# Kernel tuning notes

Measured on AMD Instinct MI355X. Metric: run time of the kernel, lower is better.

Reference implementation:

```python
import jax, jax.numpy as jnp
import numpy as np

TREND_SCALING = 0.6
DETAIL_PRESERVATION = 0.85
SPIKE_THRESHOLD = 3.5
SPIKE_DAMPING = 0.35
ITERATIONS = 2
BASE_WINDOW = 5
STRIDE = max(1, BASE_WINDOW // 2)  # 2
R = BASE_WINDOW                    # 5
EPS = 1e-6


def setup_inputs() -> dict:
    key = jax.random.key(0)
    B, C, L = 4, 4, 1048576
    x = jax.random.normal(key, (B, C, L), dtype=jnp.float32)
    # registered buffers: normalized box kernels (1/window)
    detail_kernel = jnp.ones((1, 1, BASE_WINDOW), jnp.float32) / float(BASE_WINDOW)
    trend_kernel = jnp.ones((1, 1, BASE_WINDOW * 2 + 1), jnp.float32) / float(BASE_WINDOW * 2 + 1)
    return {"x": x, "detail_kernel": detail_kernel, "trend_kernel": trend_kernel}


def _smooth(x, kernel):
    # depthwise (grouped) conv1d with reflect padding, same length out
    pad = kernel.shape[-1] // 2
    xp = jnp.pad(x, ((0, 0), (0, 0), (pad, pad)), mode="reflect")
    C = x.shape[1]
    w = jnp.broadcast_to(kernel, (C, 1, kernel.shape[-1]))
    return jax.lax.conv_general_dilated(
        xp, w, window_strides=(1,), padding="VALID",
        dimension_numbers=("NCH", "OIH", "NCH"), feature_group_count=C)


def _denoise_pass(x, detail_kernel, trend_kernel):
    B, C, L = x.shape
    trend = _smooth(x, trend_kernel)
    local = _smooth(x, detail_kernel)
    residual = x - local
    # torch .std() is unbiased (ddof=1)
    scale = jnp.maximum(jnp.std(residual, axis=-1, keepdims=True, ddof=1), EPS)
    threshold = scale * SPIKE_THRESHOLD
    residual = jnp.where(jnp.abs(residual) > threshold, residual * SPIKE_DAMPING, residual)
    residual = residual * DETAIL_PRESERVATION
    blended = (1.0 - TREND_SCALING) * local + TREND_SCALING * trend
    xp = blended + residual

    remainder = (L - R) % STRIDE
    pad_right = 0 if remainder == 0 else STRIDE - remainder
    if pad_right > 0:
        xp = jnp.pad(xp, ((0, 0), (0, 0), (0, pad_right)), mode="reflect")
    L_pad = xp.shape[-1]

    # overlap-add scatter-mean (faithful to torch unfold + scatter_add_ + count)
    n_ranges = (L_pad - R) // STRIDE + 1
    starts = jnp.arange(n_ranges) * STRIDE                      # [N]
    idx = (starts[:, None] + jnp.arange(R)[None, :]).reshape(-1)  # [N*R]
    xf = xp.reshape(B * C, L_pad)
    segments = xf[:, idx]                                       # [BC, N*R] unfold windows
    out = jnp.zeros((B * C, L_pad), xf.dtype).at[:, idx].add(segments)
    count = jnp.zeros((L_pad,), xf.dtype).at[idx].add(1.0)
    out = out / jnp.maximum(count, 1.0)[None, :]
    return out.reshape(B, C, L_pad)[:, :, :L]


def reference(x, detail_kernel, trend_kernel):
    cur = x.astype(jnp.float32)
    for _ in range(ITERATIONS):
        cur = _denoise_pass(cur, detail_kernel, trend_kernel)
    return cur.astype(x.dtype)
```

## Files before the change

### kernel.cpp

```cpp
#include <hip/hip_runtime.h>

#define NTHREADS 256
#define EPT      8
#define CHUNK    (NTHREADS*EPT)
#define ROWS     16
#define BPRB     64
#define NBLOCKS  (ROWS*BPRB)

#define C_TREND   0.6f
#define C_DETAIL  0.85f
#define C_SPIKE_T 3.5f
#define C_SPIKE_D 0.35f
#define C_EPS     1e-6f

typedef float vfloat4 __attribute__((ext_vector_type(4)));

__device__ __forceinline__ float reflect_load(const float* __restrict__ rp, int g, int L) {
    if (g < 0) g = -g;
    else if (g >= L) g = 2 * L - 2 - g;
    return rp[g];
}

__device__ __forceinline__ void blk_reduce2(double& s, double& s2) {
    #pragma unroll
    for (int off = 32; off > 0; off >>= 1) {
        s  += __shfl_xor(s, off);
        s2 += __shfl_xor(s2, off);
    }
    __shared__ double lds[8];
    int wid = threadIdx.x >> 6, lane = threadIdx.x & 63;
    if (lane == 0) { lds[2*wid] = s; lds[2*wid+1] = s2; }
    __syncthreads();
    s  = lds[0] + lds[2] + lds[4] + lds[6];
    s2 = lds[1] + lds[3] + lds[5] + lds[7];
}

__device__ __forceinline__ float compute_thr(const double2* __restrict__ prow, int L) {
    __shared__ float thr_s;
    if (threadIdx.x < 64) {
        double2 v = prow[threadIdx.x];
        double s = v.x, s2 = v.y;
        #pragma unroll
        for (int off = 32; off > 0; off >>= 1) {
            s  += __shfl_xor(s, off);
            s2 += __shfl_xor(s2, off);
        }
        if (threadIdx.x == 0) {
            double n = (double)L;
            double var = (s2 - s * s / n) / (n - 1.0);
            float stdv = (float)sqrt(fmax(var, 0.0));
            thr_s = fmaxf(stdv, C_EPS) * C_SPIKE_T;
        }
    }
    __syncthreads();
    return thr_s;
}

__device__ float xp1_scalar(const float* __restrict__ rp, int L, int p, float thr) {
    if (p < 0) p = -p;
    else if (p >= L) p = 2 * L - 2 - p;
    float s5 = 0.f, s11 = 0.f;
    #pragma unroll
    for (int k = -5; k <= 5; ++k) {
        float v = reflect_load(rp, p + k, L);
        s11 += v;
        if (k >= -2 && k <= 2) s5 += v;
    }
    float local = s5 * 0.2f;
    float trend = s11 * (1.0f / 11.0f);
    float r = rp[p] - local;
    r = (fabsf(r) > thr) ? r * C_SPIKE_D : r;
    return (1.0f - C_TREND) * local + C_TREND * trend + C_DETAIL * r;
}

__global__ __launch_bounds__(NTHREADS) void k1_reduce(
    const float* __restrict__ x, double2* __restrict__ partials1, int L, int cpb) {
    int row = blockIdx.x / BPRB, cgid = blockIdx.x % BPRB;
    const float* rp = x + (size_t)row * L;
    int base = cgid * cpb;

    double s = 0.0, s2 = 0.0;
    for (int i = 0; i < cpb; ++i) {
        int o = (base + i) * CHUNK + threadIdx.x * EPT;
        float w[16];
        if (o >= 4 && o + 12 <= L) {
            const float4* p = reinterpret_cast<const float4*>(rp + o - 4);
            #pragma unroll
            for (int j = 0; j < 4; ++j) {
                float4 v = p[j];
                w[4*j+0] = v.x; w[4*j+1] = v.y; w[4*j+2] = v.z; w[4*j+3] = v.w;
            }
        } else {
            #pragma unroll
            for (int j = 0; j < 16; ++j) w[j] = reflect_load(rp, o - 4 + j, L);
        }
        float s5 = w[2] + w[3] + w[4] + w[5] + w[6];
        #pragma unroll
        for (int k = 0; k < EPT; ++k) {
            float r = w[4 + k] - s5 * 0.2f;
            s += (double)r;
            s2 = fma((double)r, (double)r, s2);
            if (k < EPT - 1) s5 += w[7 + k] - w[2 + k];
        }
    }
    blk_reduce2(s, s2);
    if (threadIdx.x == 0) partials1[blockIdx.x] = make_double2(s, s2);
}

__global__ __launch_bounds__(NTHREADS) void k2_reduce(
    const float* __restrict__ x, const double2* __restrict__ partials1,
    double2* __restrict__ partials2, int L, int cpb) {
    int row = blockIdx.x / BPRB, cgid = blockIdx.x % BPRB;
    const float* rp = x + (size_t)row * L;
    float t1 = compute_thr(partials1 + row * BPRB, L);
    int base = cgid * cpb;

    double s = 0.0, s2 = 0.0;
    for (int i = 0; i < cpb; ++i) {
        int o = (base + i) * CHUNK + threadIdx.x * EPT;
        float xv[12];
        if (o >= 8 && o + 16 <= L) {
            float w[24];
            const float4* p = reinterpret_cast<const float4*>(rp + o - 8);
            #pragma unroll
            for (int j = 0; j < 6; ++j) {
                float4 v = p[j];
                w[4*j+0] = v.x; w[4*j+1] = v.y; w[4*j+2] = v.z; w[4*j+3] = v.w;
            }
            float s5  = w[4] + w[5] + w[6] + w[7] + w[8];
            float s11 = w[1] + w[2] + w[3] + w[4] + w[5] + w[6]
                      + w[7] + w[8] + w[9] + w[10] + w[11];
            #pragma unroll
            for (int j = 0; j < 12; ++j) {
                float local = s5 * 0.2f;
                float trend = s11 * (1.0f / 11.0f);
                float r = w[6 + j] - local;
                r = (fabsf(r) > t1) ? r * C_SPIKE_D : r;
                xv[j] = (1.0f - C_TREND) * local + C_TREND * trend + C_DETAIL * r;
                if (j < 11) { s5 += w[9 + j] - w[4 + j]; s11 += w[12 + j] - w[1 + j]; }
            }
        } else {
            #pragma unroll
            for (int j = 0; j < 12; ++j) xv[j] = xp1_scalar(rp, L, o - 2 + j, t1);
        }
        float t5 = xv[0] + xv[1] + xv[2] + xv[3] + xv[4];
        #pragma unroll
        for (int k = 0; k < EPT; ++k) {
            float r2 = xv[2 + k] - t5 * 0.2f;
            s += (double)r2;
            s2 = fma((double)r2, (double)r2, s2);
            if (k < EPT - 1) t5 += xv[5 + k] - xv[k];
        }
    }
    blk_reduce2(s, s2);
    if (threadIdx.x == 0) partials2[blockIdx.x] = make_double2(s, s2);
}

__global__ __launch_bounds__(NTHREADS) void k3_apply(
    const float* __restrict__ x, const double2* __restrict__ partials1,
    const double2* __restrict__ partials2, float* __restrict__ out, int L, int cpb) {
    int row = blockIdx.x / BPRB, cgid = blockIdx.x % BPRB;
    const float* rp = x + (size_t)row * L;
    float* orow = out + (size_t)row * L;
    float t1 = compute_thr(partials1 + row * BPRB, L);
    float t2 = compute_thr(partials2 + row * BPRB, L);
    int base = cgid * cpb;

    for (int i = 0; i < cpb; ++i) {
        int o = (base + i) * CHUNK + threadIdx.x * EPT;
        float xv[18];
        if (o >= 12 && o + 20 <= L) {
            float w[32];
            const float4* p = reinterpret_cast<const float4*>(rp + o - 12);
            #pragma unroll
            for (int j = 0; j < 8; ++j) {
                float4 v = p[j];
                w[4*j+0] = v.x; w[4*j+1] = v.y; w[4*j+2] = v.z; w[4*j+3] = v.w;
            }
            float s5  = w[5] + w[6] + w[7] + w[8] + w[9];
            float s11 = w[2] + w[3] + w[4] + w[5] + w[6] + w[7]
                      + w[8] + w[9] + w[10] + w[11] + w[12];
            #pragma unroll
            for (int j = 0; j < 18; ++j) {
                float local = s5 * 0.2f;
                float trend = s11 * (1.0f / 11.0f);
                float r = w[7 + j] - local;
                r = (fabsf(r) > t1) ? r * C_SPIKE_D : r;
                xv[j] = (1.0f - C_TREND) * local + C_TREND * trend + C_DETAIL * r;
                if (j < 17) { s5 += w[10 + j] - w[5 + j]; s11 += w[13 + j] - w[2 + j]; }
            }
        } else {
            #pragma unroll
            for (int j = 0; j < 18; ++j) xv[j] = xp1_scalar(rp, L, o - 5 + j, t1);
        }

        float s5  = xv[3] + xv[4] + xv[5] + xv[6] + xv[7];
        float s11 = xv[0] + xv[1] + xv[2] + xv[3] + xv[4] + xv[5]
                  + xv[6] + xv[7] + xv[8] + xv[9] + xv[10];
        float res[EPT];
        #pragma unroll
        for (int k = 0; k < EPT; ++k) {
            float local = s5 * 0.2f;
            float trend = s11 * (1.0f / 11.0f);
            float r = xv[5 + k] - local;
            r = (fabsf(r) > t2) ? r * C_SPIKE_D : r;
            res[k] = (1.0f - C_TREND) * local + C_TREND * trend + C_DETAIL * r;
            if (k < EPT - 1) { s5 += xv[8 + k] - xv[3 + k]; s11 += xv[11 + k] - xv[k]; }
        }
        vfloat4 r0 = { res[0], res[1], res[2], res[3] };
        vfloat4 r1 = { res[4], res[5], res[6], res[7] };
        __builtin_nontemporal_store(r0, reinterpret_cast<vfloat4*>(orow + o));
        __builtin_nontemporal_store(r1, reinterpret_cast<vfloat4*>(orow + o) + 1);
    }
}

extern "C" void kernel_launch(void* const* d_in, const int* in_sizes, int n_in,
                              void* d_out, int out_size, void* d_ws, size_t ws_size,
                              hipStream_t stream) {
    const float* x = (const float*)d_in[0];
    float* outp = (float*)d_out;

    int total = in_sizes[0];
    int L = total / ROWS;
    int bpr = L / CHUNK;
    int cpb = bpr / BPRB;

    double2* partials1 = (double2*)d_ws;
    double2* partials2 = partials1 + NBLOCKS;

    k1_reduce<<<NBLOCKS, NTHREADS, 0, stream>>>(x, partials1, L, cpb);
    k2_reduce<<<NBLOCKS, NTHREADS, 0, stream>>>(x, partials1, partials2, L, cpb);
    k3_apply <<<NBLOCKS, NTHREADS, 0, stream>>>(x, partials1, partials2, outp, L, cpb);
}
```

Measured before the change: 70.82 us.

## Fuse three passes into one cooperative kernel with grid-wide syncs

Replaces the three separate launches (two statistics reductions and the apply pass) with a single cooperative kernel of 512 blocks that uses grid.sync between phases, with the three-kernel path kept as a fallback. Partials are exchanged through relaxed agent-scope atomic loads and stores. The aim is to remove launch gaps and inter-kernel drain/fill costs. In exchange it runs half as many blocks, each with more chunks, and pays for grid barriers and an occupancy query on every launch.

```diff
diff --git a/kernel.cpp b/kernel.cpp
--- a/kernel.cpp
+++ b/kernel.cpp
@@ -1,11 +1,16 @@
 #include <hip/hip_runtime.h>
+#include <hip/hip_cooperative_groups.h>
+
+namespace cg = cooperative_groups;
 
 #define NTHREADS 256
 #define EPT      8
 #define CHUNK    (NTHREADS*EPT)
 #define ROWS     16
-#define BPRB     64
-#define NBLOCKS  (ROWS*BPRB)
+#define NBLOCKS_C 512
+#define BPRB_C   (NBLOCKS_C/ROWS)
+#define NBLOCKS_F 1024
+#define BPRB_F   (NBLOCKS_F/ROWS)
 
 #define C_TREND   0.6f
 #define C_DETAIL  0.85f
@@ -29,19 +34,28 @@
     }
     __shared__ double lds[8];
     int wid = threadIdx.x >> 6, lane = threadIdx.x & 63;
+    __syncthreads();
     if (lane == 0) { lds[2*wid] = s; lds[2*wid+1] = s2; }
     __syncthreads();
     s  = lds[0] + lds[2] + lds[4] + lds[6];
     s2 = lds[1] + lds[3] + lds[5] + lds[7];
 }
 
-__device__ __forceinline__ float compute_thr(const double2* __restrict__ prow, int L) {
+template<int NPART, bool ATOMIC>
+__device__ __forceinline__ float compute_thr(const double* __restrict__ prow, int L) {
     __shared__ float thr_s;
-    if (threadIdx.x < 64) {
-        double2 v = prow[threadIdx.x];
-        double s = v.x, s2 = v.y;
-        #pragma unroll
-        for (int off = 32; off > 0; off >>= 1) {
+    __syncthreads();
+    if (threadIdx.x < NPART) {
+        double s, s2;
+        if (ATOMIC) {
+            s  = __hip_atomic_load(prow + 2*threadIdx.x + 0, __ATOMIC_RELAXED, __HIP_MEMORY_SCOPE_AGENT);
+            s2 = __hip_atomic_load(prow + 2*threadIdx.x + 1, __ATOMIC_RELAXED, __HIP_MEMORY_SCOPE_AGENT);
+        } else {
+            s  = prow[2*threadIdx.x + 0];
+            s2 = prow[2*threadIdx.x + 1];
+        }
+        #pragma unroll
+        for (int off = NPART/2; off > 0; off >>= 1) {
             s  += __shfl_xor(s, off);
             s2 += __shfl_xor(s2, off);
         }
@@ -73,145 +87,194 @@
     return (1.0f - C_TREND) * local + C_TREND * trend + C_DETAIL * r;
 }
 
+
+__device__ __forceinline__ void chunkA(const float* __restrict__ rp, int o, int L,
+                                       double& s, double& s2) {
+    float w[16];
+    if (o >= 4 && o + 12 <= L) {
+        const float4* p = reinterpret_cast<const float4*>(rp + o - 4);
+        #pragma unroll
+        for (int j = 0; j < 4; ++j) {
+            float4 v = p[j];
+            w[4*j+0] = v.x; w[4*j+1] = v.y; w[4*j+2] = v.z; w[4*j+3] = v.w;
+        }
+    } else {
+        #pragma unroll
+        for (int j = 0; j < 16; ++j) w[j] = reflect_load(rp, o - 4 + j, L);
+    }
+    float s5 = w[2] + w[3] + w[4] + w[5] + w[6];
+    #pragma unroll
+    for (int k = 0; k < EPT; ++k) {
+        float r = w[4 + k] - s5 * 0.2f;
+        s += (double)r;
+        s2 = fma((double)r, (double)r, s2);
+        if (k < EPT - 1) s5 += w[7 + k] - w[2 + k];
+    }
+}
+
+__device__ __forceinline__ void chunkB(const float* __restrict__ rp, int o, int L,
+                                       float t1, double& s, double& s2) {
+    float xv[12];
+    if (o >= 8 && o + 16 <= L) {
+        float w[24];
+        const float4* p = reinterpret_cast<const float4*>(rp + o - 8);
+        #pragma unroll
+        for (int j = 0; j < 6; ++j) {
+            float4 v = p[j];
+            w[4*j+0] = v.x; w[4*j+1] = v.y; w[4*j+2] = v.z; w[4*j+3] = v.w;
+        }
+        float s5  = w[4] + w[5] + w[6] + w[7] + w[8];
+        float s11 = w[1] + w[2] + w[3] + w[4] + w[5] + w[6]
+                  + w[7] + w[8] + w[9] + w[10] + w[11];
+        #pragma unroll
+        for (int j = 0; j < 12; ++j) {
+            float local = s5 * 0.2f;
+            float trend = s11 * (1.0f / 11.0f);
+            float r = w[6 + j] - local;
+            r = (fabsf(r) > t1) ? r * C_SPIKE_D : r;
+            xv[j] = (1.0f - C_TREND) * local + C_TREND * trend + C_DETAIL * r;
+            if (j < 11) { s5 += w[9 + j] - w[4 + j]; s11 += w[12 + j] - w[1 + j]; }
+        }
+    } else {
+        #pragma unroll
+        for (int j = 0; j < 12; ++j) xv[j] = xp1_scalar(rp, L, o - 2 + j, t1);
+    }
+    float t5 = xv[0] + xv[1] + xv[2] + xv[3] + xv[4];
+    #pragma unroll
+    for (int k = 0; k < EPT; ++k) {
+        float r2 = xv[2 + k] - t5 * 0.2f;
+        s += (double)r2;
+        s2 = fma((double)r2, (double)r2, s2);
+        if (k < EPT - 1) t5 += xv[5 + k] - xv[k];
+    }
+}
+
+__device__ __forceinline__ void chunkC(const float* __restrict__ rp, float* __restrict__ orow,
+                                       int o, int L, float t1, float t2) {
+    float xv[18];
+    if (o >= 12 && o + 20 <= L) {
+        float w[32];
+        const float4* p = reinterpret_cast<const float4*>(rp + o - 12);
+        #pragma unroll
+        for (int j = 0; j < 8; ++j) {
+            float4 v = p[j];
+            w[4*j+0] = v.x; w[4*j+1] = v.y; w[4*j+2] = v.z; w[4*j+3] = v.w;
+        }
+        float s5  = w[5] + w[6] + w[7] + w[8] + w[9];
+        float s11 = w[2] + w[3] + w[4] + w[5] + w[6] + w[7]
+                  + w[8] + w[9] + w[10] + w[11] + w[12];
+        #pragma unroll
+        for (int j = 0; j < 18; ++j) {
+            float local = s5 * 0.2f;
+            float trend = s11 * (1.0f / 11.0f);
+            float r = w[7 + j] - local;
+            r = (fabsf(r) > t1) ? r * C_SPIKE_D : r;
+            xv[j] = (1.0f - C_TREND) * local + C_TREND * trend + C_DETAIL * r;
+            if (j < 17) { s5 += w[10 + j] - w[5 + j]; s11 += w[13 + j] - w[2 + j]; }
+        }
+    } else {
+        #pragma unroll
+        for (int j = 0; j < 18; ++j) xv[j] = xp1_scalar(rp, L, o - 5 + j, t1);
+    }
+    float s5  = xv[3] + xv[4] + xv[5] + xv[6] + xv[7];
+    float s11 = xv[0] + xv[1] + xv[2] + xv[3] + xv[4] + xv[5]
+              + xv[6] + xv[7] + xv[8] + xv[9] + xv[10];
+    float res[EPT];
+    #pragma unroll
+    for (int k = 0; k < EPT; ++k) {
+        float local = s5 * 0.2f;
+        float trend = s11 * (1.0f / 11.0f);
+        float r = xv[5 + k] - local;
+        r = (fabsf(r) > t2) ? r * C_SPIKE_D : r;
+        res[k] = (1.0f - C_TREND) * local + C_TREND * trend + C_DETAIL * r;
+        if (k < EPT - 1) { s5 += xv[8 + k] - xv[3 + k]; s11 += xv[11 + k] - xv[k]; }
+    }
+    vfloat4 r0 = { res[0], res[1], res[2], res[3] };
+    vfloat4 r1 = { res[4], res[5], res[6], res[7] };
+    __builtin_nontemporal_store(r0, reinterpret_cast<vfloat4*>(orow + o));
+    __builtin_nontemporal_store(r1, reinterpret_cast<vfloat4*>(orow + o) + 1);
+}
+
+__global__ __launch_bounds__(NTHREADS) void fractal_coop(
+    const float* __restrict__ x, float* __restrict__ out,
+    double* __restrict__ p1, double* __restrict__ p2, int L) {
+    cg::grid_group grid = cg::this_grid();
+    int row  = blockIdx.x / BPRB_C;
+    int cgid = blockIdx.x % BPRB_C;
+    int cpb  = (L / CHUNK) / BPRB_C;
+    const float* rp = x + (size_t)row * L;
+    float* orow = out + (size_t)row * L;
+    int base = cgid * cpb;
+
+    {
+        double s = 0.0, s2 = 0.0;
+        for (int i = 0; i < cpb; ++i)
+            chunkA(rp, (base + i) * CHUNK + threadIdx.x * EPT, L, s, s2);
+        blk_reduce2(s, s2);
+        if (threadIdx.x == 0) {
+            __hip_atomic_store(p1 + 2*blockIdx.x + 0, s,  __ATOMIC_RELAXED, __HIP_MEMORY_SCOPE_AGENT);
+            __hip_atomic_store(p1 + 2*blockIdx.x + 1, s2, __ATOMIC_RELAXED, __HIP_MEMORY_SCOPE_AGENT);
+        }
+    }
+    grid.sync();
+
+    float t1 = compute_thr<BPRB_C, true>(p1 + row * 2 * BPRB_C, L);
+
+    {
+        double s = 0.0, s2 = 0.0;
+        for (int i = 0; i < cpb; ++i)
+            chunkB(rp, (base + i) * CHUNK + threadIdx.x * EPT, L, t1, s, s2);
+        blk_reduce2(s, s2);
+        if (threadIdx.x == 0) {
+            __hip_atomic_store(p2 + 2*blockIdx.x + 0, s,  __ATOMIC_RELAXED, __HIP_MEMORY_SCOPE_AGENT);
+            __hip_atomic_store(p2 + 2*blockIdx.x + 1, s2, __ATOMIC_RELAXED, __HIP_MEMORY_SCOPE_AGENT);
+        }
+    }
+    grid.sync();
+
+    float t2 = compute_thr<BPRB_C, true>(p2 + row * 2 * BPRB_C, L);
+
+    for (int i = 0; i < cpb; ++i)
+        chunkC(rp, orow, (base + i) * CHUNK + threadIdx.x * EPT, L, t1, t2);
+}
+
 __global__ __launch_bounds__(NTHREADS) void k1_reduce(
-    const float* __restrict__ x, double2* __restrict__ partials1, int L, int cpb) {
-    int row = blockIdx.x / BPRB, cgid = blockIdx.x % BPRB;
+    const float* __restrict__ x, double* __restrict__ partials1, int L, int cpb) {
+    int row = blockIdx.x / BPRB_F, cgid = blockIdx.x % BPRB_F;
     const float* rp = x + (size_t)row * L;
     int base = cgid * cpb;
-
     double s = 0.0, s2 = 0.0;
-    for (int i = 0; i < cpb; ++i) {
-        int o = (base + i) * CHUNK + threadIdx.x * EPT;
-        float w[16];
-        if (o >= 4 && o + 12 <= L) {
-            const float4* p = reinterpret_cast<const float4*>(rp + o - 4);
-            #pragma unroll
-            for (int j = 0; j < 4; ++j) {
-                float4 v = p[j];
-                w[4*j+0] = v.x; w[4*j+1] = v.y; w[4*j+2] = v.z; w[4*j+3] = v.w;
-            }
-        } else {
-            #pragma unroll
-            for (int j = 0; j < 16; ++j) w[j] = reflect_load(rp, o - 4 + j, L);
-        }
-        float s5 = w[2] + w[3] + w[4] + w[5] + w[6];
-        #pragma unroll
-        for (int k = 0; k < EPT; ++k) {
-            float r = w[4 + k] - s5 * 0.2f;
-            s += (double)r;
-            s2 = fma((double)r, (double)r, s2);
-            if (k < EPT - 1) s5 += w[7 + k] - w[2 + k];
-        }
-    }
+    for (int i = 0; i < cpb; ++i)
+        chunkA(rp, (base + i) * CHUNK + threadIdx.x * EPT, L, s, s2);
     blk_reduce2(s, s2);
-    if (threadIdx.x == 0) partials1[blockIdx.x] = make_double2(s, s2);
+    if (threadIdx.x == 0) { partials1[2*blockIdx.x] = s; partials1[2*blockIdx.x+1] = s2; }
 }
 
 __global__ __launch_bounds__(NTHREADS) void k2_reduce(
-    const float* __restrict__ x, const double2* __restrict__ partials1,
-    double2* __restrict__ partials2, int L, int cpb) {
-    int row = blockIdx.x / BPRB, cgid = blockIdx.x % BPRB;
+    const float* __restrict__ x, const double* __restrict__ partials1,
+    double* __restrict__ partials2, int L, int cpb) {
+    int row = blockIdx.x / BPRB_F, cgid = blockIdx.x % BPRB_F;
     const float* rp = x + (size_t)row * L;
-    float t1 = compute_thr(partials1 + row * BPRB, L);
+    float t1 = compute_thr<BPRB_F, false>(partials1 + row * 2 * BPRB_F, L);
     int base = cgid * cpb;
-
     double s = 0.0, s2 = 0.0;
-    for (int i = 0; i < cpb; ++i) {
-        int o = (base + i) * CHUNK + threadIdx.x * EPT;
-        float xv[12];
-        if (o >= 8 && o + 16 <= L) {
-            float w[24];
-            const float4* p = reinterpret_cast<const float4*>(rp + o - 8);
-            #pragma unroll
-            for (int j = 0; j < 6; ++j) {
-                float4 v = p[j];
-                w[4*j+0] = v.x; w[4*j+1] = v.y; w[4*j+2] = v.z; w[4*j+3] = v.w;
-            }
-            float s5  = w[4] + w[5] + w[6] + w[7] + w[8];
-            float s11 = w[1] + w[2] + w[3] + w[4] + w[5] + w[6]
-                      + w[7] + w[8] + w[9] + w[10] + w[11];
-            #pragma unroll
-            for (int j = 0; j < 12; ++j) {
-                float local = s5 * 0.2f;
-                float trend = s11 * (1.0f / 11.0f);
-                float r = w[6 + j] - local;
-                r = (fabsf(r) > t1) ? r * C_SPIKE_D : r;
-                xv[j] = (1.0f - C_TREND) * local + C_TREND * trend + C_DETAIL * r;
-                if (j < 11) { s5 += w[9 + j] - w[4 + j]; s11 += w[12 + j] - w[1 + j]; }
-            }
-        } else {
-            #pragma unroll
-            for (int j = 0; j < 12; ++j) xv[j] = xp1_scalar(rp, L, o - 2 + j, t1);
-        }
-        float t5 = xv[0] + xv[1] + xv[2] + xv[3] + xv[4];
-        #pragma unroll
-        for (int k = 0; k < EPT; ++k) {
-            float r2 = xv[2 + k] - t5 * 0.2f;
-            s += (double)r2;
-            s2 = fma((double)r2, (double)r2, s2);
-            if (k < EPT - 1) t5 += xv[5 + k] - xv[k];
-        }
-    }
+    for (int i = 0; i < cpb; ++i)
+        chunkB(rp, (base + i) * CHUNK + threadIdx.x * EPT, L, t1, s, s2);
     blk_reduce2(s, s2);
-    if (threadIdx.x == 0) partials2[blockIdx.x] = make_double2(s, s2);
+    if (threadIdx.x == 0) { partials2[2*blockIdx.x] = s; partials2[2*blockIdx.x+1] = s2; }
 }
 
 __global__ __launch_bounds__(NTHREADS) void k3_apply(
-    const float* __restrict__ x, const double2* __restrict__ partials1,
-    const double2* __restrict__ partials2, float* __restrict__ out, int L, int cpb) {
-    int row = blockIdx.x / BPRB, cgid = blockIdx.x % BPRB;
+    const float* __restrict__ x, const double* __restrict__ partials1,
+    const double* __restrict__ partials2, float* __restrict__ out, int L, int cpb) {
+    int row = blockIdx.x / BPRB_F, cgid = blockIdx.x % BPRB_F;
     const float* rp = x + (size_t)row * L;
     float* orow = out + (size_t)row * L;
-    float t1 = compute_thr(partials1 + row * BPRB, L);
-    float t2 = compute_thr(partials2 + row * BPRB, L);
+    float t1 = compute_thr<BPRB_F, false>(partials1 + row * 2 * BPRB_F, L);
+    float t2 = compute_thr<BPRB_F, false>(partials2 + row * 2 * BPRB_F, L);
     int base = cgid * cpb;
-
-    for (int i = 0; i < cpb; ++i) {
-        int o = (base + i) * CHUNK + threadIdx.x * EPT;
-        float xv[18];
-        if (o >= 12 && o + 20 <= L) {
-            float w[32];
-            const float4* p = reinterpret_cast<const float4*>(rp + o - 12);
-            #pragma unroll
-            for (int j = 0; j < 8; ++j) {
-                float4 v = p[j];
-                w[4*j+0] = v.x; w[4*j+1] = v.y; w[4*j+2] = v.z; w[4*j+3] = v.w;
-            }
-            float s5  = w[5] + w[6] + w[7] + w[8] + w[9];
-            float s11 = w[2] + w[3] + w[4] + w[5] + w[6] + w[7]
-                      + w[8] + w[9] + w[10] + w[11] + w[12];
-            #pragma unroll
-            for (int j = 0; j < 18; ++j) {
-                float local = s5 * 0.2f;
-                float trend = s11 * (1.0f / 11.0f);
-                float r = w[7 + j] - local;
-                r = (fabsf(r) > t1) ? r * C_SPIKE_D : r;
-                xv[j] = (1.0f - C_TREND) * local + C_TREND * trend + C_DETAIL * r;
-                if (j < 17) { s5 += w[10 + j] - w[5 + j]; s11 += w[13 + j] - w[2 + j]; }
-            }
-        } else {
-            #pragma unroll
-            for (int j = 0; j < 18; ++j) xv[j] = xp1_scalar(rp, L, o - 5 + j, t1);
-        }
-
-        float s5  = xv[3] + xv[4] + xv[5] + xv[6] + xv[7];
-        float s11 = xv[0] + xv[1] + xv[2] + xv[3] + xv[4] + xv[5]
-                  + xv[6] + xv[7] + xv[8] + xv[9] + xv[10];
-        float res[EPT];
-        #pragma unroll
-        for (int k = 0; k < EPT; ++k) {
-            float local = s5 * 0.2f;
-            float trend = s11 * (1.0f / 11.0f);
-            float r = xv[5 + k] - local;
-            r = (fabsf(r) > t2) ? r * C_SPIKE_D : r;
-            res[k] = (1.0f - C_TREND) * local + C_TREND * trend + C_DETAIL * r;
-            if (k < EPT - 1) { s5 += xv[8 + k] - xv[3 + k]; s11 += xv[11 + k] - xv[k]; }
-        }
-        vfloat4 r0 = { res[0], res[1], res[2], res[3] };
-        vfloat4 r1 = { res[4], res[5], res[6], res[7] };
-        __builtin_nontemporal_store(r0, reinterpret_cast<vfloat4*>(orow + o));
-        __builtin_nontemporal_store(r1, reinterpret_cast<vfloat4*>(orow + o) + 1);
-    }
+    for (int i = 0; i < cpb; ++i)
+        chunkC(rp, orow, (base + i) * CHUNK + threadIdx.x * EPT, L, t1, t2);
 }
 
 extern "C" void kernel_launch(void* const* d_in, const int* in_sizes, int n_in,
@@ -222,13 +285,25 @@
 
     int total = in_sizes[0];
     int L = total / ROWS;
-    int bpr = L / CHUNK;
-    int cpb = bpr / BPRB;
-
-    double2* partials1 = (double2*)d_ws;
-    double2* partials2 = partials1 + NBLOCKS;
-
-    k1_reduce<<<NBLOCKS, NTHREADS, 0, stream>>>(x, partials1, L, cpb);
-    k2_reduce<<<NBLOCKS, NTHREADS, 0, stream>>>(x, partials1, partials2, L, cpb);
-    k3_apply <<<NBLOCKS, NTHREADS, 0, stream>>>(x, partials1, partials2, outp, L, cpb);
-}
+
+    double* p1c = (double*)d_ws;
+    double* p2c = p1c + 2 * NBLOCKS_C;
+    double* p1f = p2c + 2 * NBLOCKS_C;
+    double* p2f = p1f + 2 * NBLOCKS_F;
+
+    int maxBlk = 0;
+    hipError_t qe = hipOccupancyMaxActiveBlocksPerMultiprocessor(
+        &maxBlk, (const void*)fractal_coop, NTHREADS, 0);
+    bool coop = (qe == hipSuccess) && (maxBlk * 256 >= NBLOCKS_C);
+    if (coop) {
+        void* args[] = { (void*)&x, (void*)&outp, (void*)&p1c, (void*)&p2c, (void*)&L };
+        coop = (hipLaunchCooperativeKernel((void*)fractal_coop, dim3(NBLOCKS_C),
+                                           dim3(NTHREADS), args, 0, stream) == hipSuccess);
+    }
+    if (!coop) {
+        int cpb = (L / CHUNK) / BPRB_F;
+        k1_reduce<<<NBLOCKS_F, NTHREADS, 0, stream>>>(x, p1f, L, cpb);
+        k2_reduce<<<NBLOCKS_F, NTHREADS, 0, stream>>>(x, p1f, p2f, L, cpb);
+        k3_apply <<<NBLOCKS_F, NTHREADS, 0, stream>>>(x, p1f, p2f, outp, L, cpb);
+    }
+}
```

After: 184.0 us. 160% more time.
